# Kernel tuning notes

Hardware: AMD Instinct MI355X
Metric: run time of the kernel (lower is better)

The kernel has to match this reference:

```python
import jax, jax.numpy as jnp
import numpy as np


def setup_inputs() -> dict:
    key = jax.random.key(0)
    B, C, H, W = 16, 128, 64, 64
    k = 3
    x = jax.random.normal(key, (B, C, H, W), dtype=jnp.float32)
    # Fixed identity 'im2col' kernel: eye(k*k) -> (k*k, 1, k, k), non-trainable buffer.
    weights = jnp.eye(k * k, dtype=jnp.float32).reshape(k * k, 1, k, k)
    return {"x": x, "weights": weights}


def reference(x, weights):
    B, C, H, W = x.shape
    k = weights.shape[-1]  # kernel_size
    pad = k // 2
    # Treat every (b, c) plane as an independent single-channel image.
    xr = x.reshape(B * C, 1, H, W)
    # Eye-weighted conv == unfold: each of the k*k output channels is a shifted copy.
    y = jax.lax.conv_general_dilated(
        xr, weights,
        window_strides=(1, 1),
        padding=((pad, pad), (pad, pad)),
        dimension_numbers=("NCHW", "OIHW", "NCHW"),
    )  # (B*C, k*k, H, W)
    return y.reshape(B, C * k * k, H * W)
```

## Files before the change

kernel.cpp:

```cpp
#include <hip/hip_runtime.h>


#define S 67
#define LDS_ELEMS (66 * S)

typedef float f32x4 __attribute__((ext_vector_type(4)));

__global__ __launch_bounds__(256) void unfold_kernel(
    const float* __restrict__ x, float* __restrict__ y) {
    __shared__ float lds[LDS_ELEMS];
    const int j  = threadIdx.x;
    const int bc = blockIdx.x;

    const f32x4* plane = (const f32x4*)(x + ((size_t)bc << 12));
    f32x4 v0 = plane[j];
    f32x4 v1 = plane[256 + j];
    f32x4 v2 = plane[512 + j];
    f32x4 v3 = plane[768 + j];

    if (j < S) {
        lds[j] = 0.f;
        lds[65 * S + j] = 0.f;
    }
    if (j < 64) {
        lds[(j + 1) * S] = 0.f;
        lds[(j + 1) * S + 65] = 0.f;
    }

    #pragma unroll
    for (int q = 0; q < 4; ++q) {
        f32x4 v = (q == 0) ? v0 : (q == 1) ? v1 : (q == 2) ? v2 : v3;
        int f = q * 256 + j;
        int h = f >> 4;
        int w = (f & 15) << 2;
        float* dst = &lds[(h + 1) * S + (w + 1)];
        dst[0] = v.x; dst[1] = v.y; dst[2] = v.z; dst[3] = v.w;
    }
    __syncthreads();

    float* ybase = y + ((size_t)bc * 9 << 12);
    #pragma unroll
    for (int t = 0; t < 9; ++t) {
        const int dh = t / 3 - 1;
        const int dw = t % 3 - 1;
        f32x4* yt = (f32x4*)(ybase + ((size_t)t << 12));
        #pragma unroll
        for (int q = 0; q < 4; ++q) {
            int f = q * 256 + j;
            int h = f >> 4;
            int w = (f & 15) << 2;
            const float* s = &lds[(h + 1 + dh) * S + (w + 1 + dw)];
            f32x4 v;
            v.x = s[0]; v.y = s[1]; v.z = s[2]; v.w = s[3];
            yt[f] = v;
        }
    }
}

extern "C" void kernel_launch(void* const* d_in, const int* in_sizes, int n_in,
                              void* d_out, int out_size, void* d_ws, size_t ws_size,
                              hipStream_t stream) {
    const float* x = (const float*)d_in[0];
    float* y = (float*)d_out;

    unfold_kernel<<<2048, 256, 0, stream>>>(x, y);
}
```

Baseline: 324.7 us.

## Replace LDS staging with register shuffles and row-shifted output stores

After: 327.2 us. No clear change (+0.8%).

```diff
diff --git a/kernel.cpp b/kernel.cpp
--- a/kernel.cpp
+++ b/kernel.cpp
@@ -1,42 +1,32 @@
 #include <hip/hip_runtime.h>
 
-
-#define S 67
-#define LDS_ELEMS (66 * S)
 
 typedef float f32x4 __attribute__((ext_vector_type(4)));
 
 __global__ __launch_bounds__(256) void unfold_kernel(
     const float* __restrict__ x, float* __restrict__ y) {
-    __shared__ float lds[LDS_ELEMS];
-    const int j  = threadIdx.x;
-    const int bc = blockIdx.x;
+    const int j      = threadIdx.x;
+    const int bc     = blockIdx.x;
+    const int lane16 = j & 15;
+    const int rowid  = j >> 4;
 
     const f32x4* plane = (const f32x4*)(x + ((size_t)bc << 12));
-    f32x4 v0 = plane[j];
-    f32x4 v1 = plane[256 + j];
-    f32x4 v2 = plane[512 + j];
-    f32x4 v3 = plane[768 + j];
+    f32x4 v[4];
+    #pragma unroll
+    for (int q = 0; q < 4; ++q) v[q] = plane[q * 256 + j];
 
-    if (j < S) {
-        lds[j] = 0.f;
-        lds[65 * S + j] = 0.f;
-    }
-    if (j < 64) {
-        lds[(j + 1) * S] = 0.f;
-        lds[(j + 1) * S + 65] = 0.f;
+    f32x4 sL[4], sR[4];
+    #pragma unroll
+    for (int q = 0; q < 4; ++q) {
+        float nxt = __shfl_down(v[q].x, 1, 16);
+        float prv = __shfl_up  (v[q].w, 1, 16);
+        nxt = (lane16 == 15) ? 0.f : nxt;
+        prv = (lane16 == 0)  ? 0.f : prv;
+        sR[q].x = v[q].y; sR[q].y = v[q].z; sR[q].z = v[q].w; sR[q].w = nxt;
+        sL[q].x = prv;    sL[q].y = v[q].x; sL[q].z = v[q].y; sL[q].w = v[q].z;
     }
 
-    #pragma unroll
-    for (int q = 0; q < 4; ++q) {
-        f32x4 v = (q == 0) ? v0 : (q == 1) ? v1 : (q == 2) ? v2 : v3;
-        int f = q * 256 + j;
-        int h = f >> 4;
-        int w = (f & 15) << 2;
-        float* dst = &lds[(h + 1) * S + (w + 1)];
-        dst[0] = v.x; dst[1] = v.y; dst[2] = v.z; dst[3] = v.w;
-    }
-    __syncthreads();
+    const f32x4 zero4 = {0.f, 0.f, 0.f, 0.f};
 
     float* ybase = y + ((size_t)bc * 9 << 12);
     #pragma unroll
@@ -46,13 +36,14 @@
         f32x4* yt = (f32x4*)(ybase + ((size_t)t << 12));
         #pragma unroll
         for (int q = 0; q < 4; ++q) {
-            int f = q * 256 + j;
-            int h = f >> 4;
-            int w = (f & 15) << 2;
-            const float* s = &lds[(h + 1 + dh) * S + (w + 1 + dw)];
-            f32x4 v;
-            v.x = s[0]; v.y = s[1]; v.z = s[2]; v.w = s[3];
-            yt[f] = v;
+            const int h    = (q << 4) + rowid;
+            const int orow = h - dh;
+            const bool valid = ((unsigned)orow) < 64u;
+            f32x4 sv = (dw == 0) ? v[q] : ((dw > 0) ? sR[q] : sL[q]);
+            f32x4 out = sv;
+            int   row = orow;
+            if (!valid) { out = zero4; row = (dh > 0) ? 63 : 0; }
+            yt[(row << 4) + lane16] = out;
         }
     }
 }
```
